# Kernel optimization log

Hardware: AMD Instinct MI355X
Metric: run time of the kernel (lower is better)

## Reference

```python
import jax, jax.numpy as jnp
import numpy as np

B, T, D, H = 4, 2048, 1024, 16
HD = D // H  # 64
FF = 4 * D


def layernorm(x, g, b, eps=1e-5):
    mu = jnp.mean(x, axis=-1, keepdims=True)
    var = jnp.mean(jnp.square(x - mu), axis=-1, keepdims=True)
    return (x - mu) * jax.lax.rsqrt(var + eps) * g + b


def setup_inputs() -> dict:
    key = jax.random.key(0)
    ks = jax.random.split(key, 12)
    s_in = 1.0 / np.sqrt(D)
    s_ff = 1.0 / np.sqrt(FF)
    return {
        "x": jax.random.normal(ks[0], (B, T, D), dtype=jnp.float32),
        "mask": jnp.tril(jnp.ones((T, T), dtype=jnp.int32)),  # causal
        "ln1_g": jnp.ones((D,), jnp.float32),
        "ln1_b": jnp.zeros((D,), jnp.float32),
        "Wq": jax.random.uniform(ks[1], (H, D, HD), jnp.float32, -s_in, s_in),
        "bq": jnp.zeros((H, HD), jnp.float32),
        "Wk": jax.random.uniform(ks[2], (H, D, HD), jnp.float32, -s_in, s_in),
        "bk": jnp.zeros((H, HD), jnp.float32),
        "Wv": jax.random.uniform(ks[3], (H, D, HD), jnp.float32, -s_in, s_in),
        "bv": jnp.zeros((H, HD), jnp.float32),
        "Wo": jax.random.uniform(ks[4], (D, D), jnp.float32, -s_in, s_in),
        "bo": jnp.zeros((D,), jnp.float32),
        "ln2_g": jnp.ones((D,), jnp.float32),
        "ln2_b": jnp.zeros((D,), jnp.float32),
        "W1": jax.random.uniform(ks[5], (D, FF), jnp.float32, -s_in, s_in),
        "b1": jnp.zeros((FF,), jnp.float32),
        "W2": jax.random.uniform(ks[6], (FF, D), jnp.float32, -s_ff, s_ff),
        "b2": jnp.zeros((D,), jnp.float32),
    }


def reference(x, mask, ln1_g, ln1_b, Wq, bq, Wk, bk, Wv, bv, Wo, bo,
              ln2_g, ln2_b, W1, b1, W2, b2):
    # --- attention branch (dropout p=0, eval mode) ---
    h = layernorm(x, ln1_g, ln1_b)                      # [B,T,D]
    q = jnp.einsum('btd,hdk->bhtk', h, Wq) + bq[:, None, :]
    k = jnp.einsum('btd,hdk->bhtk', h, Wk) + bk[:, None, :]
    v = jnp.einsum('btd,hdk->bhtk', h, Wv) + bv[:, None, :]
    scores = jnp.einsum('bhqk,bhsk->bhqs', q, k) / jnp.sqrt(jnp.float32(HD))
    scores = jnp.where(mask == 0, -jnp.inf, scores)     # [B,H,T,T]
    attn = jax.nn.softmax(scores, axis=-1)
    ctx = jnp.einsum('bhqs,bhsk->bhqk', attn, v)        # [B,H,T,HD]
    # concat heads along feature dim (head order preserved)
    ctx = jnp.transpose(ctx, (0, 2, 1, 3)).reshape(x.shape[0], x.shape[1], D)
    attn_out = ctx @ Wo + bo
    x = x + attn_out
    # --- GELU FFN branch (torch nn.GELU default = exact erf) ---
    h2 = layernorm(x, ln2_g, ln2_b)
    ff = jax.nn.gelu(h2 @ W1 + b1, approximate=False) @ W2 + b2
    return x + ff
```

## Files before the change

### kernel.cpp

```cpp
#include <hip/hip_runtime.h>
#include <cstdint>
#include <cstddef>

typedef __bf16 bf16x8 __attribute__((ext_vector_type(8)));
typedef float  floatx4 __attribute__((ext_vector_type(4)));
typedef uint16_t u16x8 __attribute__((ext_vector_type(8)));

__device__ __forceinline__ uint16_t f2b(float f) {
    uint32_t u = __builtin_bit_cast(uint32_t, f);
    return (uint16_t)((u + 0x7fffu + ((u >> 16) & 1)) >> 16);
}

__device__ __forceinline__ uint16_t bf16bits(float f) {
    __bf16 h = (__bf16)f;
    return __builtin_bit_cast(uint16_t, h);
}

__device__ __forceinline__ void gload_lds16(const void* g, void* l) {
    __builtin_amdgcn_global_load_lds(
        (__attribute__((address_space(1))) void*)(void*)g,
        (__attribute__((address_space(3))) void*)l, 16, 0, 0);
}

#define QSCALE 0.18033688011112042f

__global__ __launch_bounds__(256) void repack_qkv(
    const float* __restrict__ Wq, const float* __restrict__ Wk,
    const float* __restrict__ Wv, uint16_t* __restrict__ out)
{
    __shared__ uint16_t tile[32][33];
    const int m = blockIdx.z >> 4, h = blockIdx.z & 15;
    const float* W = (m == 0) ? Wq : (m == 1) ? Wk : Wv;
    const float scl = (m == 0) ? QSCALE : 1.0f;
    const float* src = W + (size_t)h * 1024 * 64;
    const int d0 = blockIdx.x * 32, hd0 = blockIdx.y * 32;
    const int tx = threadIdx.x & 31, ty = threadIdx.x >> 5;
#pragma unroll
    for (int i = 0; i < 4; ++i)
        tile[ty + i * 8][tx] = f2b(src[(size_t)(d0 + ty + i * 8) * 64 + hd0 + tx] * scl);
    __syncthreads();
    uint16_t* dst = out + (size_t)(m * 1024 + h * 64) * 1024;
#pragma unroll
    for (int i = 0; i < 4; ++i)
        dst[(size_t)(hd0 + ty + i * 8) * 1024 + d0 + tx] = tile[tx][ty + i * 8];
}

__device__ __forceinline__ void transpose_tile_f2b(
    const float* __restrict__ in, uint16_t* __restrict__ out,
    int R, int C, int c0, int r0, int tx, int ty)
{
    __shared__ uint16_t tile[32][33];
#pragma unroll
    for (int i = 0; i < 4; ++i)
        tile[ty + i * 8][tx] = f2b(in[(size_t)(r0 + ty + i * 8) * C + c0 + tx]);
    __syncthreads();
#pragma unroll
    for (int i = 0; i < 4; ++i)
        out[(size_t)(c0 + ty + i * 8) * R + r0 + tx] = tile[tx][ty + i * 8];
}

__global__ __launch_bounds__(256) void prep_weights(
    const float* __restrict__ Wo, const float* __restrict__ W1,
    const float* __restrict__ W2,
    const float* __restrict__ bq, const float* __restrict__ bk,
    const float* __restrict__ bv,
    uint16_t* __restrict__ Wo_t, uint16_t* __restrict__ W1_t,
    uint16_t* __restrict__ W2_t, float* __restrict__ bqkv)
{
    const int bid = blockIdx.x;
    const int tx = threadIdx.x & 31, ty = threadIdx.x >> 5;
    if (bid < 1024) {
        const int bx = bid & 31, by = bid >> 5;
        transpose_tile_f2b(Wo, Wo_t, 1024, 1024, bx * 32, by * 32, tx, ty);
    } else if (bid < 1024 + 4096) {
        const int t = bid - 1024;
        const int bx = t & 127, by = t >> 7;
        transpose_tile_f2b(W1, W1_t, 1024, 4096, bx * 32, by * 32, tx, ty);
    } else if (bid < 1024 + 8192) {
        const int t = bid - 5120;
        const int bx = t & 31, by = t >> 5;
        transpose_tile_f2b(W2, W2_t, 4096, 1024, bx * 32, by * 32, tx, ty);
    } else {
        const int i = (bid - 9216) * 256 + (int)threadIdx.x;
        bqkv[i] = (i < 1024) ? bq[i] * QSCALE
                : (i < 2048) ? bk[i - 1024] : bv[i - 2048];
    }
}

__global__ __launch_bounds__(256) void ln_bf16(
    const float* __restrict__ x, const float* __restrict__ g,
    const float* __restrict__ b, uint16_t* __restrict__ out)
{
    const int row = blockIdx.x;
    const int t = threadIdx.x;
    const float4 v = ((const float4*)(x + (size_t)row * 1024))[t];
    float s  = v.x + v.y + v.z + v.w;
    float s2 = v.x * v.x + v.y * v.y + v.z * v.z + v.w * v.w;
#pragma unroll
    for (int o = 32; o > 0; o >>= 1) { s += __shfl_down(s, o); s2 += __shfl_down(s2, o); }
    __shared__ float red[8];
    const int wave = t >> 6, lane = t & 63;
    if (lane == 0) { red[wave] = s; red[4 + wave] = s2; }
    __syncthreads();
    if (t == 0) {
        float a  = red[0] + red[1] + red[2] + red[3];
        float a2 = red[4] + red[5] + red[6] + red[7];
        float mu = a * (1.0f / 1024.0f);
        red[0] = mu;
        red[4] = rsqrtf(a2 * (1.0f / 1024.0f) - mu * mu + 1e-5f);
    }
    __syncthreads();
    const float mu = red[0], rs = red[4];
    const float4 gv = ((const float4*)g)[t];
    const float4 bv = ((const float4*)b)[t];
    ushort4 ov;
    ov.x = f2b((v.x - mu) * rs * gv.x + bv.x);
    ov.y = f2b((v.y - mu) * rs * gv.y + bv.y);
    ov.z = f2b((v.z - mu) * rs * gv.z + bv.z);
    ov.w = f2b((v.w - mu) * rs * gv.w + bv.w);
    ((ushort4*)(out + (size_t)row * 1024))[t] = ov;
}

__global__ __launch_bounds__(256, 3) void gemm_bf16(
    const uint16_t* __restrict__ A, const uint16_t* __restrict__ Bt,
    int M, int N, int K,
    const float* __restrict__ bias, const float* __restrict__ resid,
    float* __restrict__ outF, uint16_t* __restrict__ outB, int mode)
{
    __shared__ __align__(16) uint16_t lds[128 * 128];
    uint16_t* lA = lds;
    uint16_t* lB = lds + 128 * 64;
    const int tid  = threadIdx.x;
    const int wave = tid >> 6, lane = tid & 63;

    const int lid = (int)blockIdx.y * (int)gridDim.x + (int)blockIdx.x;
    const int xcd = lid & 7, t = lid >> 3;
    const int Mb = (M >> 7) >> 3;
    const int perChunk = Mb * 8;
    const int ch = t / perChunk, j = t - ch * perChunk;
    const int m0 = (xcd * Mb + (j & (Mb - 1))) * 128;
    const int n0 = (ch * 8 + (j / Mb)) * 128;

    const int wm = (wave >> 1) * 64, wn = (wave & 1) * 64;
    const int quad = lane >> 4, lrow = lane & 15;
    const int wbase = wave * 64;

    floatx4 acc[4][4] = {};

    const uint16_t* aT = A  + (size_t)m0 * K;
    const uint16_t* bT = Bt + (size_t)n0 * K;

    for (int k0 = 0; k0 < K; k0 += 64) {
        __syncthreads();
#pragma unroll
        for (int i = 0; i < 4; ++i) {
            const int cw = i * 256 + wbase;
            const int q  = cw + lane;
            const int row = q >> 3;
            const int g = ((q & 7) ^ (row & 7)) * 8;
            gload_lds16(aT + (size_t)row * K + k0 + g, &lA[cw * 8]);
            gload_lds16(bT + (size_t)row * K + k0 + g, &lB[cw * 8]);
        }
        __syncthreads();
        bf16x8 af[4][2], bfr[4][2];
#pragma unroll
        for (int mi = 0; mi < 4; ++mi) {
            const int rr = wm + mi * 16 + lrow;
#pragma unroll
            for (int hh = 0; hh < 2; ++hh)
                af[mi][hh] = *(const bf16x8*)
                    &lA[rr * 64 + (((hh * 4 + quad) ^ (rr & 7)) * 8)];
        }
#pragma unroll
        for (int ni = 0; ni < 4; ++ni) {
            const int rr = wn + ni * 16 + lrow;
#pragma unroll
            for (int hh = 0; hh < 2; ++hh)
                bfr[ni][hh] = *(const bf16x8*)
                    &lB[rr * 64 + (((hh * 4 + quad) ^ (rr & 7)) * 8)];
        }
#pragma unroll
        for (int mi = 0; mi < 4; ++mi)
#pragma unroll
            for (int ni = 0; ni < 4; ++ni) {
                acc[mi][ni] = __builtin_amdgcn_mfma_f32_16x16x32_bf16(
                    af[mi][0], bfr[ni][0], acc[mi][ni], 0, 0, 0);
                acc[mi][ni] = __builtin_amdgcn_mfma_f32_16x16x32_bf16(
                    af[mi][1], bfr[ni][1], acc[mi][ni], 0, 0, 0);
            }
    }

    __syncthreads();
    const int r0 = (lane >> 4) * 4;

    if (mode == 1) {
        float* cf = (float*)lds;
#pragma unroll
        for (int p = 0; p < 2; ++p) {
            if ((wave >> 1) == p) {
#pragma unroll
                for (int ni = 0; ni < 4; ++ni) {
                    const int col = wn + ni * 16 + lrow;
                    const float bv = bias[n0 + col];
#pragma unroll
                    for (int mi = 0; mi < 4; ++mi)
#pragma unroll
                        for (int r = 0; r < 4; ++r) {
                            const int row = mi * 16 + r0 + r;
                            const int g = (col >> 2) ^ (((row >> 2) & 1) << 2);
                            cf[row * 128 + g * 4 + (col & 3)] = acc[mi][ni][r] + bv;
                        }
                }
            }
            __syncthreads();
#pragma unroll
            for (int i = 0; i < 8; ++i) {
                const int ci = i * 256 + tid;
                const int row = ci >> 5, cg = ci & 31;
                const int g = cg ^ (((row >> 2) & 1) << 2);
                float4 v = *(const float4*)&cf[row * 128 + g * 4];
                const size_t gidx = (size_t)(m0 + p * 64 + row) * N + n0 + cg * 4;
                const float4 rz = *(const float4*)&resid[gidx];
                v.x += rz.x; v.y += rz.y; v.z += rz.z; v.w += rz.w;
                *(float4*)&outF[gidx] = v;
            }
            __syncthreads();
        }
    } else {
#pragma unroll
        for (int ni = 0; ni < 4; ++ni) {
            const int col = wn + ni * 16 + lrow;
            const float bv = bias[n0 + col];
#pragma unroll
            for (int mi = 0; mi < 4; ++mi)
#pragma unroll
                for (int r = 0; r < 4; ++r) {
                    const int row = wm + mi * 16 + r0 + r;
                    float v = acc[mi][ni][r] + bv;
                    if (mode == 2)
                        v = 0.5f * v * (1.0f + erff(v * 0.70710678118654752f));
                    const int g = (col >> 3) ^ (((row >> 2) & 3) << 1);
                    lds[row * 128 + g * 8 + (col & 7)] = bf16bits(v);
                }
        }
        __syncthreads();
#pragma unroll
        for (int i = 0; i < 8; ++i) {
            const int ci = i * 256 + tid;
            const int row = ci >> 4, cg = ci & 15;
            const int g = cg ^ (((row >> 2) & 3) << 1);
            const bf16x8 v = *(const bf16x8*)&lds[row * 128 + g * 8];
            *(bf16x8*)&outB[(size_t)(m0 + row) * N + n0 + cg * 8] = v;
        }
    }
}

#define BAR()   __builtin_amdgcn_s_barrier()
#define LWAIT() asm volatile("s_waitcnt lgkmcnt(0)")
#define GWAIT(N_) asm volatile("s_waitcnt vmcnt(" #N_ ")")

#define STAGE_HALF(SRC, DSTBASE, HALF, TILE)                                    \
    { _Pragma("unroll")                                                         \
      for (int _i = 0; _i < 2; ++_i) {                                          \
        const int _q = _i * 512 + tid, _r = _q >> 3, _c = _q & 7;               \
        gload_lds16(SRC + (size_t)((HALF) * 128 + _r) * K + (TILE) * 64         \
                        + ((_c ^ (_r & 7)) * 8),                                \
                    (DSTBASE) + (HALF) * 8192 + (_i * 512 + (wave << 6)) * 8);  \
      } }

#define TILE_BODY(TT, CUR)                                                      \
  { const int _t = (TT);                                                        \
    uint16_t* const lA  = sm + (CUR) * 16384;                                   \
    uint16_t* const lB  = sm + 32768 + (CUR) * 16384;                           \
    uint16_t* const lAn = sm + (1 - (CUR)) * 16384;                             \
                                                                   \
    _Pragma("unroll")                                                           \
    for (int mi = 0; mi < 4; ++mi) {                                            \
      const int rr = arow + mi * 16;                                            \
      af[mi][0] = *(const bf16x8*)&lA[rr * 64 + c0];                            \
      af[mi][1] = *(const bf16x8*)&lA[rr * 64 + c1];                            \
    }                                                                           \
    _Pragma("unroll")                                                           \
    for (int ni = 0; ni < 4; ++ni) {                                            \
      const int rb = brow + ni * 16;                                            \
      bfr[ni][0] = *(const bf16x8*)&lB[rb * 64 + c0];                           \
      bfr[ni][1] = *(const bf16x8*)&lB[rb * 64 + c1];                           \
    }                                                                           \
    if (_t + 1 < NT) { STAGE_HALF(aT, lAn, 1, _t + 1); }                        \
    BAR(); LWAIT();                                                             \
    __builtin_amdgcn_s_setprio(1);                                              \
    _Pragma("unroll")                                                           \
    for (int mi = 0; mi < 4; ++mi)                                              \
      _Pragma("unroll")                                                         \
      for (int ni = 0; ni < 2; ++ni) {                                          \
        acc[mi][ni] = __builtin_amdgcn_mfma_f32_16x16x32_bf16(                  \
            af[mi][0], bfr[ni][0], acc[mi][ni], 0, 0, 0);                       \
        acc[mi][ni] = __builtin_amdgcn_mfma_f32_16x16x32_bf16(                  \
            af[mi][1], bfr[ni][1], acc[mi][ni], 0, 0, 0);                       \
      }                                                                         \
    __builtin_amdgcn_s_setprio(0);                                              \
    BAR();                                                                      \
                                                                   \
    if (_t + 2 < NT) { STAGE_HALF(bT, lB, 0, _t + 2); }                         \
    BAR();                                                                      \
    __builtin_amdgcn_s_setprio(1);                                              \
    _Pragma("unroll")                                                           \
    for (int mi = 0; mi < 4; ++mi)                                              \
      _Pragma("unroll")                                                         \
      for (int ni = 2; ni < 4; ++ni) {                                          \
        acc[mi][ni] = __builtin_amdgcn_mfma_f32_16x16x32_bf16(                  \
            af[mi][0], bfr[ni][0], acc[mi][ni], 0, 0, 0);                       \
        acc[mi][ni] = __builtin_amdgcn_mfma_f32_16x16x32_bf16(                  \
            af[mi][1], bfr[ni][1], acc[mi][ni], 0, 0, 0);                       \
      }                                                                         \
    __builtin_amdgcn_s_setprio(0);                                              \
    BAR();                                                                      \
                                                                   \
    _Pragma("unroll")                                                           \
    for (int mi = 0; mi < 4; ++mi) {                                            \
      const int rr = arow + 64 + mi * 16;                                       \
      af[mi][0] = *(const bf16x8*)&lA[rr * 64 + c0];                            \
      af[mi][1] = *(const bf16x8*)&lA[rr * 64 + c1];                            \
    }                                                                           \
    if (_t + 2 < NT) { STAGE_HALF(bT, lB, 1, _t + 2); }                         \
    BAR(); LWAIT();                                                             \
    __builtin_amdgcn_s_setprio(1);                                              \
    _Pragma("unroll")                                                           \
    for (int mi = 0; mi < 4; ++mi)                                              \
      _Pragma("unroll")                                                         \
      for (int ni = 0; ni < 2; ++ni) {                                          \
        acc[mi + 4][ni] = __builtin_amdgcn_mfma_f32_16x16x32_bf16(              \
            af[mi][0], bfr[ni][0], acc[mi + 4][ni], 0, 0, 0);                   \
        acc[mi + 4][ni] = __builtin_amdgcn_mfma_f32_16x16x32_bf16(              \
            af[mi][1], bfr[ni][1], acc[mi + 4][ni], 0, 0, 0);                   \
      }                                                                         \
    __builtin_amdgcn_s_setprio(0);                                              \
    BAR();                                                                      \
                                                                   \
    if (_t + 2 < NT) { STAGE_HALF(aT, lA, 0, _t + 2); }                         \
    BAR();                                                                      \
    __builtin_amdgcn_s_setprio(1);                                              \
    _Pragma("unroll")                                                           \
    for (int mi = 0; mi < 4; ++mi)                                              \
      _Pragma("unroll")                                                         \
      for (int ni = 2; ni < 4; ++ni) {                                          \
        acc[mi + 4][ni] = __builtin_amdgcn_mfma_f32_16x16x32_bf16(              \
            af[mi][0], bfr[ni][0], acc[mi + 4][ni], 0, 0, 0);                   \
        acc[mi + 4][ni] = __builtin_amdgcn_mfma_f32_16x16x32_bf16(              \
            af[mi][1], bfr[ni][1], acc[mi + 4][ni], 0, 0, 0);                   \
      }                                                                         \
    __builtin_amdgcn_s_setprio(0);                                              \
    if (_t + 2 < NT) { GWAIT(6); } else { GWAIT(0); }                           \
    BAR();                                                                      \
  }

template<int GELU, int VOUT>
__global__ __launch_bounds__(512, 2) void gemm256(
    const uint16_t* __restrict__ A, const uint16_t* __restrict__ Bt,
    int M, int N, int K,
    const float* __restrict__ bias, uint16_t* __restrict__ outB,
    uint16_t* __restrict__ VtOut)
{
    (void)M;
    __shared__ __align__(16) uint16_t sm[65536];
    const int tid  = threadIdx.x;
    const int wave = tid >> 6, lane = tid & 63;
    const int quad = lane >> 4, lcol = lane & 15, sx = lcol & 7;
    const int wm = wave >> 2, wn = wave & 3;

    const int nwg = (int)gridDim.x;
    const int q8  = nwg >> 3;
    const int wg  = ((int)blockIdx.x & 7) * q8 + ((int)blockIdx.x >> 3);
    const int ntn = N >> 8;
    const int tm = wg / ntn, tn = wg - tm * ntn;
    const int m0 = tm * 256, n0 = tn * 256;

    const uint16_t* aT = A  + (size_t)m0 * K;
    const uint16_t* bT = Bt + (size_t)n0 * K;
    const int NT = K >> 6;

    const int arow = wm * 128 + lcol;
    const int brow = wn * 64  + lcol;
    const int c0 = (quad ^ sx) * 8, c1 = ((quad + 4) ^ sx) * 8;

    floatx4 acc[8][4] = {};
    bf16x8 af[4][2], bfr[4][2];

    uint16_t* const lA0 = sm;
    uint16_t* const lA1 = sm + 16384;
    uint16_t* const lB0 = sm + 32768;
    uint16_t* const lB1 = sm + 49152;

    STAGE_HALF(bT, lB0, 0, 0);
    STAGE_HALF(bT, lB0, 1, 0);
    STAGE_HALF(aT, lA0, 0, 0);
    STAGE_HALF(aT, lA0, 1, 0);
    GWAIT(4);
    STAGE_HALF(bT, lB1, 0, 1);
    STAGE_HALF(bT, lB1, 1, 1);
    STAGE_HALF(aT, lA1, 0, 1);
    GWAIT(6);
    BAR();

    for (int t = 0; t < NT; t += 2) {
        TILE_BODY(t, 0);
        TILE_BODY(t + 1, 1);
    }

#pragma unroll
    for (int ni = 0; ni < 4; ++ni) {
        const int col = wn * 64 + ni * 16 + lcol;
        const float bv = bias[n0 + col];
#pragma unroll
        for (int mi = 0; mi < 8; ++mi)
#pragma unroll
            for (int r = 0; r < 4; ++r) {
                const int row = wm * 128 + mi * 16 + quad * 4 + r;
                float v = acc[mi][ni][r] + bv;
                if (GELU)
                    v = 0.5f * v * (1.0f + erff(v * 0.70710678118654752f));
                const int g = (col >> 3) ^ (((row >> 2) & 3) << 1);
                sm[row * 256 + g * 8 + (col & 7)] = bf16bits(v);
            }
    }
    __syncthreads();

    if (VOUT && n0 >= 2048) {
        const int bb = m0 >> 11, trow = m0 & 2047;
        const int c = tid & 255, half = tid >> 8;
        uint16_t* vrow = VtOut +
            (size_t)(bb * 1024 + (n0 - 2048) + c) * 2048 + trow;
#pragma unroll
        for (int gg = 0; gg < 2; ++gg) {
            const int grp = half * 2 + gg;
#pragma unroll
            for (int qp = 0; qp < 8; ++qp) {
                u16x8 w;
#pragma unroll
                for (int e = 0; e < 8; ++e) {
                    const int q = 2 * qp + (e >> 2), j = e & 3;
                    const int row = grp * 64 + q + 16 * j;
                    const int g = (c >> 3) ^ (((row >> 2) & 3) << 1);
                    w[e] = sm[row * 256 + g * 8 + (c & 7)];
                }
                *(u16x8*)&vrow[grp * 64 + qp * 8] = w;
            }
        }
    } else {
#pragma unroll
        for (int it = 0; it < 16; ++it) {
            const int ci = it * 512 + tid;
            const int row = ci >> 5, cg = ci & 31;
            const int g = cg ^ (((row >> 2) & 3) << 1);
            const bf16x8 v = *(const bf16x8*)&sm[row * 256 + g * 8];
            *(bf16x8*)&outB[(size_t)(m0 + row) * N + n0 + cg * 8] = v;
        }
    }
}

#undef TILE_BODY
#undef STAGE_HALF

__global__ __launch_bounds__(256, 2) void attn_kernel(
    const uint16_t* __restrict__ qkv, const uint16_t* __restrict__ Vt,
    uint16_t* __restrict__ ctx)
{
    const int h = blockIdx.y, b = blockIdx.z;
    const int tid = threadIdx.x, wave = tid >> 6, lane = tid & 63;
    const int quad = lane >> 4, lcol = lane & 15, lr4 = quad * 4;
    const int sx = lcol & 7;
    const uint16_t* qbase = qkv + (size_t)b * 2048 * 3072;
    const uint16_t* kgb = qbase + 1024 + h * 64;
    const uint16_t* vtb = Vt + (size_t)(b * 16 + h) * 64 * 2048;

    __shared__ __align__(16) uint16_t kbuf[2][64 * 64];
    __shared__ __align__(16) uint16_t vbuf[2][80 * 64];
    __shared__ __align__(16) uint16_t pshm[4][32 * 64];

    const int rr = lane >> 3, sl = lane & 7;
    const int swz = sl ^ rr;

    {
        const int buf = tid >> 7;
        const int off = (tid & 127) * 8;
        const int r64 = off >> 6;
        const uint16_t val = (r64 == 0) ? (uint16_t)0x3F80 : (uint16_t)0;
        ushort4 vv; vv.x = vv.y = vv.z = vv.w = val;
        ushort4* dst = (ushort4*)&vbuf[buf][(64 + r64) * 64 + (off & 63)];
        dst[0] = vv; dst[1] = vv;
    }

#define STAGE(ktile, bb)                                                        \
    {                                                                           \
        const int _kb = (ktile) * 64;                                           \
        _Pragma("unroll")                                                       \
        for (int i = 0; i < 2; ++i) {                                           \
            const int j = wave * 2 + i;                                         \
            const int r = j * 8 + rr;                                           \
            gload_lds16(kgb + (size_t)(_kb + r) * 3072 + swz * 8,               \
                        &kbuf[bb][j * 512]);                                    \
            gload_lds16(vtb + (size_t)r * 2048 + _kb + swz * 8,                 \
                        &vbuf[bb][j * 512]);                                    \
        }                                                                       \
    }

    for (int pp = 0; pp < 2; ++pp) {
        const int qt = pp ? (int)blockIdx.x : 15 - (int)blockIdx.x;
        const int qr0 = qt * 128 + wave * 32;

        bf16x8 qf[2][2];
#pragma unroll
        for (int mi = 0; mi < 2; ++mi) {
            const uint16_t* qp = qbase + (size_t)(qr0 + mi * 16 + lcol) * 3072 + h * 64;
            qf[mi][0] = *(const bf16x8*)(qp + quad * 8);
            qf[mi][1] = *(const bf16x8*)(qp + 32 + quad * 8);
        }

        floatx4 o[2][5] = {};

        const int nk = 2 * qt + 2;
        __syncthreads();
        STAGE(0, 0);
        int cur = 0;

        for (int kt = 0; kt < nk; ++kt) {
            const int kb = kt * 64;
            __syncthreads();
            if (kt + 1 < nk) STAGE(kt + 1, cur ^ 1);

            if (kb <= qr0 + 31) {
                bf16x8 kf[4][2];
#pragma unroll
                for (int nt = 0; nt < 4; ++nt) {
                    const int krow = nt * 16 + lcol;
                    kf[nt][0] = *(const bf16x8*)&kbuf[cur][krow * 64 + ((quad ^ sx) * 8)];
                    kf[nt][1] = *(const bf16x8*)&kbuf[cur][krow * 64 + (((quad + 4) ^ sx) * 8)];
                }
#pragma unroll
                for (int mi = 0; mi < 2; ++mi) {
                    floatx4 sv[4];
                    __builtin_amdgcn_s_setprio(1);
#pragma unroll
                    for (int nt = 0; nt < 4; ++nt) {
                        floatx4 s = {0.f, 0.f, 0.f, 0.f};
                        s = __builtin_amdgcn_mfma_f32_16x16x32_bf16(qf[mi][0], kf[nt][0], s, 0, 0, 0);
                        s = __builtin_amdgcn_mfma_f32_16x16x32_bf16(qf[mi][1], kf[nt][1], s, 0, 0, 0);
                        sv[nt] = s;
                    }
                    __builtin_amdgcn_s_setprio(0);
                    if (kb + 63 > qr0 + mi * 16) {
#pragma unroll
                        for (int nt = 0; nt < 4; ++nt)
#pragma unroll
                            for (int r = 0; r < 4; ++r) {
                                const int row = qr0 + mi * 16 + lr4 + r;
                                const int col = kb + nt * 16 + lcol;
                                if (col > row) sv[nt][r] = -1e30f;
                            }
                    }
#pragma unroll
                    for (int r = 0; r < 4; ++r) {
                        const int row = mi * 16 + lr4 + r;
                        const int xs = (row & 7) << 1;
                        ushort4 pw;
                        pw.x = bf16bits(__builtin_amdgcn_exp2f(sv[0][r]));
                        pw.y = bf16bits(__builtin_amdgcn_exp2f(sv[1][r]));
                        pw.z = bf16bits(__builtin_amdgcn_exp2f(sv[2][r]));
                        pw.w = bf16bits(__builtin_amdgcn_exp2f(sv[3][r]));
                        *(ushort4*)&pshm[wave][row * 64 + ((lcol ^ xs) << 2)] = pw;
                    }
                }
                bf16x8 pf[2][2];
#pragma unroll
                for (int mi = 0; mi < 2; ++mi) {
                    const int prow = mi * 16 + lcol;
                    const int xs = (prow & 7) << 1;
                    pf[mi][0] = *(const bf16x8*)
                        &pshm[wave][prow * 64 + (((2 * quad) ^ xs) << 2)];
                    pf[mi][1] = *(const bf16x8*)
                        &pshm[wave][prow * 64 + (((2 * quad + 8) ^ xs) << 2)];
                }
                __builtin_amdgcn_s_setprio(1);
#pragma unroll
                for (int ht = 0; ht < 5; ++ht) {
                    const int hd = ht * 16 + lcol;
                    const bf16x8 vf0 = *(const bf16x8*)&vbuf[cur][hd * 64 + ((quad ^ sx) * 8)];
                    const bf16x8 vf1 = *(const bf16x8*)&vbuf[cur][hd * 64 + (((quad + 4) ^ sx) * 8)];
#pragma unroll
                    for (int mi = 0; mi < 2; ++mi) {
                        o[mi][ht] = __builtin_amdgcn_mfma_f32_16x16x32_bf16(pf[mi][0], vf0, o[mi][ht], 0, 0, 0);
                        o[mi][ht] = __builtin_amdgcn_mfma_f32_16x16x32_bf16(pf[mi][1], vf1, o[mi][ht], 0, 0, 0);
                    }
                }
                __builtin_amdgcn_s_setprio(0);
            }
            cur ^= 1;
        }

#pragma unroll
        for (int mi = 0; mi < 2; ++mi)
#pragma unroll
            for (int r = 0; r < 4; ++r) {
                const float lsum = __shfl(o[mi][4][r], lane & 48);
                const float inv = 1.0f / lsum;
                const int row = mi * 16 + lr4 + r;
#pragma unroll
                for (int ht = 0; ht < 4; ++ht)
                    pshm[wave][row * 64 + ht * 16 + lcol] =
                        bf16bits(o[mi][ht][r] * inv);
            }
#pragma unroll
        for (int it = 0; it < 4; ++it) {
            const int ci = it * 64 + lane;
            const int row = ci >> 3, c8 = ci & 7;
            const bf16x8 v = *(const bf16x8*)&pshm[wave][row * 64 + c8 * 8];
            *(bf16x8*)&ctx[(size_t)(b * 2048 + qr0 + row) * 1024 + h * 64 + c8 * 8] = v;
        }
    }
#undef STAGE
}

extern "C" void kernel_launch(void* const* d_in, const int* in_sizes, int n_in,
                              void* d_out, int out_size, void* d_ws, size_t ws_size,
                              hipStream_t stream)
{
    (void)in_sizes; (void)n_in; (void)out_size; (void)ws_size;
    const float* x     = (const float*)d_in[0];
    const float* ln1_g = (const float*)d_in[2];
    const float* ln1_b = (const float*)d_in[3];
    const float* Wq    = (const float*)d_in[4];
    const float* bq    = (const float*)d_in[5];
    const float* Wk    = (const float*)d_in[6];
    const float* bk    = (const float*)d_in[7];
    const float* Wv    = (const float*)d_in[8];
    const float* bv    = (const float*)d_in[9];
    const float* Wo    = (const float*)d_in[10];
    const float* bo    = (const float*)d_in[11];
    const float* ln2_g = (const float*)d_in[12];
    const float* ln2_b = (const float*)d_in[13];
    const float* W1    = (const float*)d_in[14];
    const float* b1    = (const float*)d_in[15];
    const float* W2    = (const float*)d_in[16];
    const float* b2    = (const float*)d_in[17];
    float* out = (float*)d_out;

    char* w = (char*)d_ws;
    uint16_t* Wqkv_t = (uint16_t*)w;  w += 6291456;
    uint16_t* Wo_t   = (uint16_t*)w;  w += 2097152;
    uint16_t* W1_t   = (uint16_t*)w;  w += 8388608;
    uint16_t* W2_t   = (uint16_t*)w;  w += 8388608;
    float*    bqkv   = (float*)w;     w += 16384;
    float*    x2     = (float*)w;     w += 33554432;
    char* region = w;
    uint16_t* hbuf = (uint16_t*)region;
    uint16_t* qkv  = (uint16_t*)(region + 16777216);
    uint16_t* Vt   = (uint16_t*)(region + 16777216 + 50331648);
    uint16_t* ctx  = hbuf;
    uint16_t* h2   = (uint16_t*)region;
    uint16_t* a1   = (uint16_t*)(region + 16777216);

    repack_qkv<<<dim3(32, 2, 48), 256, 0, stream>>>(Wq, Wk, Wv, Wqkv_t);
    prep_weights<<<dim3(9228), 256, 0, stream>>>(Wo, W1, W2, bq, bk, bv,
                                                 Wo_t, W1_t, W2_t, bqkv);
    ln_bf16<<<8192, 256, 0, stream>>>(x, ln1_g, ln1_b, hbuf);
    gemm256<0, 1><<<dim3(384), 512, 0, stream>>>(hbuf, Wqkv_t, 8192, 3072, 1024,
                                                 bqkv, qkv, Vt);
    attn_kernel<<<dim3(8, 16, 4), 256, 0, stream>>>(qkv, Vt, ctx);
    gemm_bf16<<<dim3(8, 64), 256, 0, stream>>>(ctx, Wo_t, 8192, 1024, 1024,
                                               bo, x, x2, nullptr, 1);
    ln_bf16<<<8192, 256, 0, stream>>>(x2, ln2_g, ln2_b, h2);
    gemm256<1, 0><<<dim3(512), 512, 0, stream>>>(h2, W1_t, 8192, 4096, 1024,
                                                 b1, a1, nullptr);
    gemm_bf16<<<dim3(8, 64), 256, 0, stream>>>(a1, W2_t, 8192, 1024, 4096,
                                               b2, x2, out, nullptr, 1);
}
```

Measured before the change: 498.9 us.

## Load K/V fragments directly from global memory in attention, drop LDS staging

The attention kernel no longer stages K and V tiles through double-buffered LDS with async global-to-LDS loads and block barriers. Each wave now reads its K and V^T MFMA fragments straight from global memory and runs only over the key tiles its own 32 query rows need. The row-sum column is built from a register constant of ones instead of padded LDS rows. This removes block-wide syncs and the LDS traffic, at the cost of redundant global/L2 reads across the four waves and no prefetch to hide load latency.

```diff
diff --git a/kernel.cpp b/kernel.cpp
--- a/kernel.cpp
+++ b/kernel.cpp
@@ -468,40 +468,18 @@
     const int h = blockIdx.y, b = blockIdx.z;
     const int tid = threadIdx.x, wave = tid >> 6, lane = tid & 63;
     const int quad = lane >> 4, lcol = lane & 15, lr4 = quad * 4;
-    const int sx = lcol & 7;
     const uint16_t* qbase = qkv + (size_t)b * 2048 * 3072;
     const uint16_t* kgb = qbase + 1024 + h * 64;
     const uint16_t* vtb = Vt + (size_t)(b * 16 + h) * 64 * 2048;
 
-    __shared__ __align__(16) uint16_t kbuf[2][64 * 64];
-    __shared__ __align__(16) uint16_t vbuf[2][80 * 64];
     __shared__ __align__(16) uint16_t pshm[4][32 * 64];
 
-    const int rr = lane >> 3, sl = lane & 7;
-    const int swz = sl ^ rr;
-
+    bf16x8 vones;
     {
-        const int buf = tid >> 7;
-        const int off = (tid & 127) * 8;
-        const int r64 = off >> 6;
-        const uint16_t val = (r64 == 0) ? (uint16_t)0x3F80 : (uint16_t)0;
-        ushort4 vv; vv.x = vv.y = vv.z = vv.w = val;
-        ushort4* dst = (ushort4*)&vbuf[buf][(64 + r64) * 64 + (off & 63)];
-        dst[0] = vv; dst[1] = vv;
-    }
-
-#define STAGE(ktile, bb)                                                        \
-    {                                                                           \
-        const int _kb = (ktile) * 64;                                           \
-        _Pragma("unroll")                                                       \
-        for (int i = 0; i < 2; ++i) {                                           \
-            const int j = wave * 2 + i;                                         \
-            const int r = j * 8 + rr;                                           \
-            gload_lds16(kgb + (size_t)(_kb + r) * 3072 + swz * 8,               \
-                        &kbuf[bb][j * 512]);                                    \
-            gload_lds16(vtb + (size_t)r * 2048 + _kb + swz * 8,                 \
-                        &vbuf[bb][j * 512]);                                    \
-        }                                                                       \
+        const uint16_t u = (lcol == 0) ? (uint16_t)0x3F80 : (uint16_t)0;
+#pragma unroll
+        for (int e = 0; e < 8; ++e)
+            vones[e] = __builtin_bit_cast(__bf16, u);
     }
 
     for (int pp = 0; pp < 2; ++pp) {
@@ -518,83 +496,80 @@
 
         floatx4 o[2][5] = {};
 
-        const int nk = 2 * qt + 2;
-        __syncthreads();
-        STAGE(0, 0);
-        int cur = 0;
-
-        for (int kt = 0; kt < nk; ++kt) {
+        const int nkw = (qr0 + 95) >> 6;
+
+        for (int kt = 0; kt < nkw; ++kt) {
             const int kb = kt * 64;
-            __syncthreads();
-            if (kt + 1 < nk) STAGE(kt + 1, cur ^ 1);
-
-            if (kb <= qr0 + 31) {
-                bf16x8 kf[4][2];
+
+            bf16x8 kf[4][2];
+#pragma unroll
+            for (int nt = 0; nt < 4; ++nt) {
+                const uint16_t* kp = kgb + (size_t)(kb + nt * 16 + lcol) * 3072;
+                kf[nt][0] = *(const bf16x8*)(kp + quad * 8);
+                kf[nt][1] = *(const bf16x8*)(kp + 32 + quad * 8);
+            }
+#pragma unroll
+            for (int mi = 0; mi < 2; ++mi) {
+                floatx4 sv[4];
+                __builtin_amdgcn_s_setprio(1);
 #pragma unroll
                 for (int nt = 0; nt < 4; ++nt) {
-                    const int krow = nt * 16 + lcol;
-                    kf[nt][0] = *(const bf16x8*)&kbuf[cur][krow * 64 + ((quad ^ sx) * 8)];
-                    kf[nt][1] = *(const bf16x8*)&kbuf[cur][krow * 64 + (((quad + 4) ^ sx) * 8)];
-                }
-#pragma unroll
-                for (int mi = 0; mi < 2; ++mi) {
-                    floatx4 sv[4];
-                    __builtin_amdgcn_s_setprio(1);
-#pragma unroll
-                    for (int nt = 0; nt < 4; ++nt) {
-                        floatx4 s = {0.f, 0.f, 0.f, 0.f};
-                        s = __builtin_amdgcn_mfma_f32_16x16x32_bf16(qf[mi][0], kf[nt][0], s, 0, 0, 0);
-                        s = __builtin_amdgcn_mfma_f32_16x16x32_bf16(qf[mi][1], kf[nt][1], s, 0, 0, 0);
-                        sv[nt] = s;
-                    }
-                    __builtin_amdgcn_s_setprio(0);
-                    if (kb + 63 > qr0 + mi * 16) {
-#pragma unroll
-                        for (int nt = 0; nt < 4; ++nt)
-#pragma unroll
-                            for (int r = 0; r < 4; ++r) {
-                                const int row = qr0 + mi * 16 + lr4 + r;
-                                const int col = kb + nt * 16 + lcol;
-                                if (col > row) sv[nt][r] = -1e30f;
-                            }
-                    }
-#pragma unroll
-                    for (int r = 0; r < 4; ++r) {
-                        const int row = mi * 16 + lr4 + r;
-                        const int xs = (row & 7) << 1;
-                        ushort4 pw;
-                        pw.x = bf16bits(__builtin_amdgcn_exp2f(sv[0][r]));
-                        pw.y = bf16bits(__builtin_amdgcn_exp2f(sv[1][r]));
-                        pw.z = bf16bits(__builtin_amdgcn_exp2f(sv[2][r]));
-                        pw.w = bf16bits(__builtin_amdgcn_exp2f(sv[3][r]));
-                        *(ushort4*)&pshm[wave][row * 64 + ((lcol ^ xs) << 2)] = pw;
-                    }
-                }
-                bf16x8 pf[2][2];
-#pragma unroll
-                for (int mi = 0; mi < 2; ++mi) {
-                    const int prow = mi * 16 + lcol;
-                    const int xs = (prow & 7) << 1;
-                    pf[mi][0] = *(const bf16x8*)
-                        &pshm[wave][prow * 64 + (((2 * quad) ^ xs) << 2)];
-                    pf[mi][1] = *(const bf16x8*)
-                        &pshm[wave][prow * 64 + (((2 * quad + 8) ^ xs) << 2)];
-                }
-                __builtin_amdgcn_s_setprio(1);
-#pragma unroll
-                for (int ht = 0; ht < 5; ++ht) {
-                    const int hd = ht * 16 + lcol;
-                    const bf16x8 vf0 = *(const bf16x8*)&vbuf[cur][hd * 64 + ((quad ^ sx) * 8)];
-                    const bf16x8 vf1 = *(const bf16x8*)&vbuf[cur][hd * 64 + (((quad + 4) ^ sx) * 8)];
-#pragma unroll
-                    for (int mi = 0; mi < 2; ++mi) {
-                        o[mi][ht] = __builtin_amdgcn_mfma_f32_16x16x32_bf16(pf[mi][0], vf0, o[mi][ht], 0, 0, 0);
-                        o[mi][ht] = __builtin_amdgcn_mfma_f32_16x16x32_bf16(pf[mi][1], vf1, o[mi][ht], 0, 0, 0);
-                    }
+                    floatx4 s = {0.f, 0.f, 0.f, 0.f};
+                    s = __builtin_amdgcn_mfma_f32_16x16x32_bf16(qf[mi][0], kf[nt][0], s, 0, 0, 0);
+                    s = __builtin_amdgcn_mfma_f32_16x16x32_bf16(qf[mi][1], kf[nt][1], s, 0, 0, 0);
+                    sv[nt] = s;
                 }
                 __builtin_amdgcn_s_setprio(0);
-            }
-            cur ^= 1;
+                if (kb + 63 > qr0 + mi * 16) {
+#pragma unroll
+                    for (int nt = 0; nt < 4; ++nt)
+#pragma unroll
+                        for (int r = 0; r < 4; ++r) {
+                            const int row = qr0 + mi * 16 + lr4 + r;
+                            const int col = kb + nt * 16 + lcol;
+                            if (col > row) sv[nt][r] = -1e30f;
+                        }
+                }
+#pragma unroll
+                for (int r = 0; r < 4; ++r) {
+                    const int row = mi * 16 + lr4 + r;
+                    const int xs = (row & 7) << 1;
+                    ushort4 pw;
+                    pw.x = bf16bits(__builtin_amdgcn_exp2f(sv[0][r]));
+                    pw.y = bf16bits(__builtin_amdgcn_exp2f(sv[1][r]));
+                    pw.z = bf16bits(__builtin_amdgcn_exp2f(sv[2][r]));
+                    pw.w = bf16bits(__builtin_amdgcn_exp2f(sv[3][r]));
+                    *(ushort4*)&pshm[wave][row * 64 + ((lcol ^ xs) << 2)] = pw;
+                }
+            }
+            bf16x8 pf[2][2];
+#pragma unroll
+            for (int mi = 0; mi < 2; ++mi) {
+                const int prow = mi * 16 + lcol;
+                const int xs = (prow & 7) << 1;
+                pf[mi][0] = *(const bf16x8*)
+                    &pshm[wave][prow * 64 + (((2 * quad) ^ xs) << 2)];
+                pf[mi][1] = *(const bf16x8*)
+                    &pshm[wave][prow * 64 + (((2 * quad + 8) ^ xs) << 2)];
+            }
+            __builtin_amdgcn_s_setprio(1);
+#pragma unroll
+            for (int ht = 0; ht < 4; ++ht) {
+                const uint16_t* vp = vtb + (size_t)(ht * 16 + lcol) * 2048 + kb;
+                const bf16x8 vf0 = *(const bf16x8*)(vp + quad * 8);
+                const bf16x8 vf1 = *(const bf16x8*)(vp + 32 + quad * 8);
+#pragma unroll
+                for (int mi = 0; mi < 2; ++mi) {
+                    o[mi][ht] = __builtin_amdgcn_mfma_f32_16x16x32_bf16(pf[mi][0], vf0, o[mi][ht], 0, 0, 0);
+                    o[mi][ht] = __builtin_amdgcn_mfma_f32_16x16x32_bf16(pf[mi][1], vf1, o[mi][ht], 0, 0, 0);
+                }
+            }
+#pragma unroll
+            for (int mi = 0; mi < 2; ++mi) {
+                o[mi][4] = __builtin_amdgcn_mfma_f32_16x16x32_bf16(pf[mi][0], vones, o[mi][4], 0, 0, 0);
+                o[mi][4] = __builtin_amdgcn_mfma_f32_16x16x32_bf16(pf[mi][1], vones, o[mi][4], 0, 0, 0);
+            }
+            __builtin_amdgcn_s_setprio(0);
         }
 
 #pragma unroll
@@ -617,7 +592,6 @@
             *(bf16x8*)&ctx[(size_t)(b * 2048 + qr0 + row) * 1024 + h * 64 + c8 * 8] = v;
         }
     }
-#undef STAGE
 }
 
 extern "C" void kernel_launch(void* const* d_in, const int* in_sizes, int n_in,
```

Result: slower. 566.3 us (+13.5%).
